# Kernel optimization log

Measured on AMD Instinct MI355X. Metric: run time of the kernel, lower is better.

## Reference

```python
import jax, jax.numpy as jnp
import numpy as np

N = 30000      # nodes
E = 1000000    # edges
G = 256        # graphs
IN = 3         # in_channels
H = 8          # heads
D = 16         # per-head dim
HID = 128      # hidden_dim = H*D
L = 3          # num_layers
KP = 17        # num_keypoints
KPE = 16       # kp_emb_dim
NEG = 0.2      # GATv2 leaky_relu negative slope
EPS = 1e-5     # BatchNorm eps


def setup_inputs() -> dict:
    key = jax.random.key(0)
    ks = jax.random.split(key, 24)
    x = jax.random.normal(ks[0], (N, IN), jnp.float32)
    edge_index = jax.random.randint(ks[1], (2, E), 0, N, jnp.int32)
    batch = jnp.sort(jax.random.randint(ks[2], (N,), 0, G, jnp.int32))
    s_in = 1.0 / np.sqrt(IN + KPE)
    s_h = 1.0 / np.sqrt(HID)
    return {
        "x": x,
        "edge_index": edge_index,
        "batch": batch,
        "kp_emb": jax.random.normal(ks[3], (KP, KPE), jnp.float32),
        "w_in": jax.random.normal(ks[4], (IN + KPE, HID), jnp.float32) * s_in,
        "b_in": jax.random.normal(ks[5], (HID,), jnp.float32) * 0.01,
        "w_l": jax.random.normal(ks[6], (L, HID, HID), jnp.float32) * s_h,
        "w_r": jax.random.normal(ks[7], (L, HID, HID), jnp.float32) * s_h,
        "att": jax.random.normal(ks[8], (L, H, D), jnp.float32) * (1.0 / np.sqrt(D)),
        "conv_bias": jax.random.normal(ks[9], (L, HID), jnp.float32) * 0.01,
        "bn_gamma": jnp.ones((L, HID), jnp.float32) + 0.1 * jax.random.normal(ks[10], (L, HID), jnp.float32),
        "bn_beta": 0.1 * jax.random.normal(ks[11], (L, HID), jnp.float32),
        "bn_mean": 0.1 * jax.random.normal(ks[12], (L, HID), jnp.float32),
        "bn_var": 0.5 + jax.random.uniform(ks[13], (L, HID), jnp.float32),
        "w1": jax.random.normal(ks[14], (HID, 2 * HID), jnp.float32) * s_h,
        "b1": jnp.zeros((2 * HID,), jnp.float32),
        "w2": jax.random.normal(ks[15], (2 * HID, HID), jnp.float32) * (1.0 / np.sqrt(2 * HID)),
        "b2": jnp.zeros((HID,), jnp.float32),
        "w3": jax.random.normal(ks[16], (HID, 2), jnp.float32) * s_h,
        "b3": jnp.zeros((2,), jnp.float32),
    }


def reference(x, edge_index, batch, kp_emb, w_in, b_in, w_l, w_r, att, conv_bias,
              bn_gamma, bn_beta, bn_mean, bn_var, w1, b1, w2, b2, w3, b3):
    n = x.shape[0]
    # keypoint id embedding concat + input projection
    kp_ids = jnp.arange(n) % KP
    h = jnp.concatenate([x, kp_emb[kp_ids]], axis=-1) @ w_in + b_in  # [N, HID]
    # GATv2Conv adds self loops by default
    loops = jnp.arange(n, dtype=edge_index.dtype)
    src = jnp.concatenate([edge_index[0], loops])  # message sources (j)
    dst = jnp.concatenate([edge_index[1], loops])  # message targets (i)
    for l in range(L):
        xl = (h @ w_l[l]).reshape(n, H, D)  # source transform (lin_l)
        xr = (h @ w_r[l]).reshape(n, H, D)  # target transform (lin_r)
        z = xl[src] + xr[dst]                              # [Et, H, D]
        score = jnp.einsum('ehd,hd->eh', jax.nn.leaky_relu(z, NEG), att[l])
        # segment softmax over incoming edges of each dst node
        m = jax.ops.segment_max(score, dst, num_segments=n)
        ex = jnp.exp(score - m[dst])
        denom = jax.ops.segment_sum(ex, dst, num_segments=n)
        alpha = ex / denom[dst]                            # [Et, H]
        msg = xl[src] * alpha[..., None]                   # [Et, H, D]
        out = jax.ops.segment_sum(msg, dst, num_segments=n).reshape(n, HID) + conv_bias[l]
        out = jax.nn.relu(out)
        # BatchNorm1d (eval mode: running stats)
        out = (out - bn_mean[l]) * (bn_gamma[l] / jnp.sqrt(bn_var[l] + EPS)) + bn_beta[l]
        h = h + out  # residual (dropout = identity in eval)
    # global mean pool per graph
    sums = jax.ops.segment_sum(h, batch, num_segments=G)
    cnt = jax.ops.segment_sum(jnp.ones((n, 1), h.dtype), batch, num_segments=G)
    g = sums / jnp.maximum(cnt, 1.0)
    # classifier MLP
    g = jax.nn.elu(g @ w1 + b1)
    g = jax.nn.elu(g @ w2 + b2)
    return g @ w3 + b3  # [G, 2]
```

## Files before the change

### kernel.cpp

```cpp
#include <hip/hip_runtime.h>
#include <hip/hip_bf16.h>

#define N_NODES 30000
#define N_EDGES 1000000
#define N_GRAPHS 256
#define HEADS 8
#define DHEAD 16
#define HIDDEN 128
#define LAYERS 3
#define KPN 17
#define KPE 16
#define NEG_SLOPE 0.2f
#define BN_EPS 1e-5f
#define ET (N_EDGES + N_NODES)
#define NBIN 235
#define BINW 128
#define BINCAP 6144
#define CHUNK 4096
#define NB_EDGE 245
#define NB_WCONV 384
#define SRC_HALF 15000

typedef __attribute__((ext_vector_type(8))) short bf16x8;
typedef __attribute__((ext_vector_type(4))) float f32x4;

__device__ __forceinline__ unsigned bf16_rne(float f) {
    unsigned u = __float_as_uint(f);
    return (u + 0x7fffu + ((u >> 16) & 1u)) >> 16;
}

__global__ __launch_bounds__(256) void k_bin(const int* __restrict__ ei,
                                             int* __restrict__ bcnt,
                                             unsigned* __restrict__ bdata,
                                             const int* __restrict__ batch,
                                             int* __restrict__ gptr,
                                             int* __restrict__ ptr,
                                             const float* __restrict__ w_l,
                                             const float* __restrict__ w_r,
                                             unsigned short* __restrict__ wT) {
    int bid = blockIdx.x;
    if (bid < NB_EDGE) {
        __shared__ int lcnt[NBIN];
        __shared__ int lbase[NBIN];
        int base = bid * CHUNK;
        int n = N_EDGES - base; if (n > CHUNK) n = CHUNK;
        for (int i = threadIdx.x; i < NBIN; i += 256) lcnt[i] = 0;
        __syncthreads();
        for (int t = threadIdx.x; t < n; t += 256) {
            int d = ei[N_EDGES + base + t];
            atomicAdd(&lcnt[d >> 7], 1);
        }
        __syncthreads();
        for (int i = threadIdx.x; i < NBIN; i += 256) {
            int c = lcnt[i];
            lbase[i] = c ? atomicAdd(&bcnt[i], c) : 0;
            lcnt[i] = 0;
        }
        __syncthreads();
        for (int t = threadIdx.x; t < n; t += 256) {
            int s = ei[base + t];
            int d = ei[N_EDGES + base + t];
            int b = d >> 7;
            int pos = lbase[b] + atomicAdd(&lcnt[b], 1);
            bdata[(size_t)b * BINCAP + pos] = (unsigned)s | ((unsigned)(d & 127) << 15);
        }
    } else if (bid == NB_EDGE) {
        for (int g = threadIdx.x; g <= N_GRAPHS; g += 256) {
            if (g == N_GRAPHS) { gptr[g] = N_NODES; }
            else {
                int lo = 0, hi = N_NODES;
                while (lo < hi) {
                    int mid = (lo + hi) >> 1;
                    if (batch[mid] < g) lo = mid + 1; else hi = mid;
                }
                gptr[g] = lo;
            }
        }
        if (threadIdx.x == 0) ptr[N_NODES] = ET;
    } else {
        int idx = (bid - NB_EDGE - 1) * 256 + threadIdx.x;
        if (idx < LAYERS * 256 * 128) {
            int l = idx / (256 * 128);
            int rem = idx - l * 256 * 128;
            int c = rem >> 7;
            int k = rem & 127;
            float v = (c < 128) ? w_l[(size_t)l * 16384 + k * 128 + c]
                                : w_r[(size_t)l * 16384 + k * 128 + (c - 128)];
            wT[idx] = (unsigned short)bf16_rne(v);
        }
    }
}

__global__ __launch_bounds__(256) void k_place2(const int* __restrict__ bcnt,
                                                const unsigned* __restrict__ bdata,
                                                int* __restrict__ ptr,
                                                unsigned short* __restrict__ csr_src) {
    __shared__ int vsc[256];
    __shared__ int histL[BINW], histH[BINW];
    __shared__ int lowS[BINW], highS[BINW];
    __shared__ int lofsL[BINW], lofsH[BINW];
    __shared__ int bbase_sh;
    int b = blockIdx.x, tid = threadIdx.x;

    int c = 0;
    if (tid < NBIN) {
        int nodes = N_NODES - tid * BINW; if (nodes > BINW) nodes = BINW;
        c = bcnt[tid] + nodes;
    }
    vsc[tid] = c;
    __syncthreads();
    for (int off = 1; off < 256; off <<= 1) {
        int x = (tid >= off) ? vsc[tid - off] : 0;
        __syncthreads();
        vsc[tid] += x;
        __syncthreads();
    }
    if (tid == 0) bbase_sh = (b == 0) ? 0 : vsc[b - 1];

    int nNodes = N_NODES - b * BINW; if (nNodes > BINW) nNodes = BINW;
    int n = bcnt[b];
    if (tid < BINW) {
        int node = b * BINW + tid;
        int valid = tid < nNodes;
        histL[tid] = (valid && node < SRC_HALF) ? 1 : 0;
        histH[tid] = (valid && node >= SRC_HALF) ? 1 : 0;
    }
    __syncthreads();
    for (int t = tid; t < n; t += 256) {
        unsigned e = bdata[(size_t)b * BINCAP + t];
        int dl = (e >> 15) & 127;
        if ((e & 0x7fffu) < SRC_HALF) atomicAdd(&histL[dl], 1);
        else                          atomicAdd(&histH[dl], 1);
    }
    __syncthreads();
    if (tid < BINW) vsc[tid] = histL[tid] + histH[tid];
    __syncthreads();
    for (int off = 1; off < BINW; off <<= 1) {
        int x = (tid >= off && tid < BINW) ? vsc[tid - off] : 0;
        __syncthreads();
        if (tid < BINW) vsc[tid] += x;
        __syncthreads();
    }
    if (tid < BINW) {
        int tot = histL[tid] + histH[tid];
        int ns = bbase_sh + vsc[tid] - tot;
        lowS[tid] = ns;
        highS[tid] = ns + histL[tid];
        int node = b * BINW + tid;
        int isLow = node < SRC_HALF;
        if (tid < nNodes) {
            ptr[node] = ns;
            if (isLow) csr_src[ns] = (unsigned short)node;
            else       csr_src[ns + histL[tid]] = (unsigned short)node;
        }
        lofsL[tid] = (tid < nNodes && isLow) ? 1 : 0;
        lofsH[tid] = (tid < nNodes && !isLow) ? 1 : 0;
    }
    __syncthreads();
    for (int t = tid; t < n; t += 256) {
        unsigned e = bdata[(size_t)b * BINCAP + t];
        int dl = (e >> 15) & 127;
        int s = e & 0x7fffu;
        int pos = (s < SRC_HALF) ? (lowS[dl] + atomicAdd(&lofsL[dl], 1))
                                 : (highS[dl] + atomicAdd(&lofsH[dl], 1));
        csr_src[pos] = (unsigned short)s;
    }
}

template<bool FUSED>
__global__ __launch_bounds__(256) void k_gemmT(const float* __restrict__ x,
                                               const float* __restrict__ kp_emb,
                                               const float* __restrict__ w_in,
                                               const float* __restrict__ b_in,
                                               float* __restrict__ h,
                                               const unsigned short* __restrict__ hb,
                                               const unsigned short* __restrict__ wT,
                                               unsigned short* __restrict__ xlb,
                                               unsigned short* __restrict__ xrb) {
    __shared__ unsigned short hsA[32][136];
    __shared__ unsigned short st[32][264];
    int tid = threadIdx.x;
    int wave = tid >> 6, lane = tid & 63;
    int brow = blockIdx.x * 32;
    int lr = lane & 15, lk = lane >> 4;

    if (FUSED) {
        int r = tid >> 3, c16 = (tid & 7) * 16;
        int gr = brow + r;
        int gc = gr < N_NODES ? gr : 0;
        float xv0 = x[gc * 3], xv1 = x[gc * 3 + 1], xv2 = x[gc * 3 + 2];
        const float* kp = kp_emb + (gc % KPN) * KPE;
        float res[16];
#pragma unroll
        for (int q = 0; q < 16; ++q) {
            int c = c16 + q;
            float acc = b_in[c] + xv0 * w_in[c] + xv1 * w_in[128 + c] + xv2 * w_in[256 + c];
#pragma unroll
            for (int kk = 0; kk < KPE; ++kk) acc += kp[kk] * w_in[(3 + kk) * 128 + c];
            res[q] = acc;
        }
        if (gr < N_NODES) {
#pragma unroll
            for (int q = 0; q < 16; q += 4)
                *(float4*)(h + (size_t)gr * 128 + c16 + q) =
                    make_float4(res[q], res[q + 1], res[q + 2], res[q + 3]);
        }
#pragma unroll
        for (int q = 0; q < 16; ++q) hsA[r][c16 + q] = (unsigned short)bf16_rne(res[q]);
        __syncthreads();
    }

    int ar0c = brow + lr;      if (ar0c >= N_NODES) ar0c = N_NODES - 1;
    int ar1c = brow + 16 + lr; if (ar1c >= N_NODES) ar1c = N_NODES - 1;
    int c0 = wave * 64 + lr;
    const unsigned short* wb = wT + (size_t)c0 * 128 + lk * 8;

    f32x4 acc[2][4];
#pragma unroll
    for (int m = 0; m < 2; ++m)
#pragma unroll
        for (int n = 0; n < 4; ++n) acc[m][n] = (f32x4){0.f, 0.f, 0.f, 0.f};

#pragma unroll
    for (int ks = 0; ks < 4; ++ks) {
        bf16x8 a0, a1;
        if (FUSED) {
            a0 = *(const bf16x8*)&hsA[lr][lk * 8 + ks * 32];
            a1 = *(const bf16x8*)&hsA[16 + lr][lk * 8 + ks * 32];
        } else {
            a0 = *(const bf16x8*)(hb + (size_t)ar0c * 128 + lk * 8 + ks * 32);
            a1 = *(const bf16x8*)(hb + (size_t)ar1c * 128 + lk * 8 + ks * 32);
        }
#pragma unroll
        for (int nt = 0; nt < 4; ++nt) {
            bf16x8 b = *(const bf16x8*)(wb + nt * 16 * 128 + ks * 32);
            acc[0][nt] = __builtin_amdgcn_mfma_f32_16x16x32_bf16(a0, b, acc[0][nt], 0, 0, 0);
            acc[1][nt] = __builtin_amdgcn_mfma_f32_16x16x32_bf16(a1, b, acc[1][nt], 0, 0, 0);
        }
    }

    int r0 = lk * 4;
#pragma unroll
    for (int mt = 0; mt < 2; ++mt)
#pragma unroll
        for (int nt = 0; nt < 4; ++nt)
#pragma unroll
            for (int j = 0; j < 4; ++j)
                st[r0 + mt * 16 + j][c0 + nt * 16] = (unsigned short)bf16_rne(acc[mt][nt][j]);
    __syncthreads();

    int rr = tid >> 3, seg = tid & 7;
    int grow = brow + rr;
    if (grow < N_NODES) {
        uint4 v0 = *(uint4*)&st[rr][seg * 32];
        uint4 v1 = *(uint4*)&st[rr][seg * 32 + 8];
        uint4 v2 = *(uint4*)&st[rr][seg * 32 + 16];
        uint4 v3 = *(uint4*)&st[rr][seg * 32 + 24];
        unsigned short* dst = (seg < 4) ? (xlb + (size_t)grow * 128 + seg * 32)
                                        : (xrb + (size_t)grow * 128 + (seg - 4) * 32);
        *(uint4*)(dst)      = v0;
        *(uint4*)(dst + 8)  = v1;
        *(uint4*)(dst + 16) = v2;
        *(uint4*)(dst + 24) = v3;
    }
}

__global__ __launch_bounds__(256) void k_gat(const unsigned* __restrict__ xlb,
                                             const unsigned* __restrict__ xrb,
                                             const int* __restrict__ ptr,
                                             const unsigned short* __restrict__ csr_src,
                                             const float* __restrict__ att_l,
                                             const float* __restrict__ bias_l,
                                             const float* __restrict__ gamma_l,
                                             const float* __restrict__ beta_l,
                                             const float* __restrict__ mean_l,
                                             const float* __restrict__ var_l,
                                             float* __restrict__ h,
                                             unsigned short* __restrict__ hb) {
    int wid = (blockIdx.x * 256 + threadIdx.x) >> 6;
    int lane = threadIdx.x & 63;
    if (wid >= N_NODES) return;
    int i = wid;
    int grp = lane >> 5;
    int l32 = lane & 31;
    int d0 = 4 * l32;

    uint2 xw = *(const uint2*)(xrb + ((size_t)i << 6) + (l32 << 1));
    float xr0 = __uint_as_float(xw.x << 16);
    float xr1 = __uint_as_float(xw.x & 0xffff0000u);
    float xr2 = __uint_as_float(xw.y << 16);
    float xr3 = __uint_as_float(xw.y & 0xffff0000u);
    const float L2E = 1.44269504089f;
    float4 av = *(const float4*)(att_l + d0);
    av.x *= L2E; av.y *= L2E; av.z *= L2E; av.w *= L2E;
    int e0 = ptr[i], e1 = ptr[i + 1];

    float denom = 0.f, acc0 = 0.f, acc1 = 0.f, acc2 = 0.f, acc3 = 0.f;

#define LDP(KP, WREG, VREG) { \
    int eo = 2 * (KP) + grp; \
    int sr = __shfl(sv, eo); \
    VREG = eo < cnt; \
    int rw = VREG ? sr : 0; \
    WREG = *(const uint2*)(xlb + ((size_t)rw << 6) + (l32 << 1)); \
}
#define PROCP(WREG, VREG) { \
    float v0 = __uint_as_float(WREG.x << 16); \
    float v1 = __uint_as_float(WREG.x & 0xffff0000u); \
    float v2 = __uint_as_float(WREG.y << 16); \
    float v3 = __uint_as_float(WREG.y & 0xffff0000u); \
    float z0 = v0 + xr0, z1 = v1 + xr1, z2 = v2 + xr2, z3 = v3 + xr3; \
    z0 = fmaxf(z0, NEG_SLOPE * z0); \
    z1 = fmaxf(z1, NEG_SLOPE * z1); \
    z2 = fmaxf(z2, NEG_SLOPE * z2); \
    z3 = fmaxf(z3, NEG_SLOPE * z3); \
    float p = z0 * av.x + z1 * av.y + z2 * av.z + z3 * av.w; \
    p += __shfl_xor(p, 1); \
    p += __shfl_xor(p, 2); \
    float ex = VREG ? exp2f(p) : 0.f; \
    denom += ex; \
    acc0 += ex * v0; acc1 += ex * v1; acc2 += ex * v2; acc3 += ex * v3; \
}

    for (int base = e0; base < e1; base += 64) {
        int idx = base + lane;
        int sv = (idx < e1) ? (int)csr_src[idx] : 0;
        int cnt = e1 - base; if (cnt > 64) cnt = 64;
        int np = (cnt + 1) >> 1;

        uint2 w0, w1; bool b0 = false, b1 = false;
        LDP(0, w0, b0);
        if (1 < np) LDP(1, w1, b1);
        int k = 0;
        for (; k + 2 < np; k += 2) {
            uint2 n0, n1; bool c0v, c1v;
            LDP(k + 2, n0, c0v);
            LDP(k + 3, n1, c1v);
            PROCP(w0, b0); PROCP(w1, b1);
            w0 = n0; b0 = c0v; w1 = n1; b1 = c1v;
        }
        PROCP(w0, b0);
        if (k + 1 < np) PROCP(w1, b1);
    }
#undef LDP
#undef PROCP

    denom += __shfl_xor(denom, 32);
    acc0 += __shfl_xor(acc0, 32);
    acc1 += __shfl_xor(acc1, 32);
    acc2 += __shfl_xor(acc2, 32);
    acc3 += __shfl_xor(acc3, 32);

    if (grp == 0) {
        float inv = 1.f / denom;
        float4 bia = *(const float4*)(bias_l + d0);
        float4 gam = *(const float4*)(gamma_l + d0);
        float4 bet = *(const float4*)(beta_l + d0);
        float4 mea = *(const float4*)(mean_l + d0);
        float4 var = *(const float4*)(var_l + d0);
        float o0 = fmaxf(acc0 * inv + bia.x, 0.f);
        float o1 = fmaxf(acc1 * inv + bia.y, 0.f);
        float o2 = fmaxf(acc2 * inv + bia.z, 0.f);
        float o3 = fmaxf(acc3 * inv + bia.w, 0.f);
        o0 = (o0 - mea.x) * (gam.x * rsqrtf(var.x + BN_EPS)) + bet.x;
        o1 = (o1 - mea.y) * (gam.y * rsqrtf(var.y + BN_EPS)) + bet.y;
        o2 = (o2 - mea.z) * (gam.z * rsqrtf(var.z + BN_EPS)) + bet.z;
        o3 = (o3 - mea.w) * (gam.w * rsqrtf(var.w + BN_EPS)) + bet.w;
        float4 hv = *(const float4*)(h + (size_t)i * 128 + d0);
        hv.x += o0; hv.y += o1; hv.z += o2; hv.w += o3;
        *(float4*)(h + (size_t)i * 128 + d0) = hv;
        unsigned pk0 = bf16_rne(hv.x) | (bf16_rne(hv.y) << 16);
        unsigned pk1 = bf16_rne(hv.z) | (bf16_rne(hv.w) << 16);
        uint2 pk; pk.x = pk0; pk.y = pk1;
        *(uint2*)(hb + (size_t)i * 128 + d0) = pk;
    }
}

__global__ __launch_bounds__(256) void k_poolmlp(const float* __restrict__ h,
                                                 const int* __restrict__ gptr,
                                                 const float* __restrict__ w1, const float* __restrict__ b1,
                                                 const float* __restrict__ w2, const float* __restrict__ b2,
                                                 const float* __restrict__ w3, const float* __restrict__ b3,
                                                 float* __restrict__ out) {
    __shared__ float red[256];
    __shared__ float g[128], t1[256], t2[128];
    int b = blockIdx.x, t = threadIdx.x;
    int c = t & 127, half = t >> 7;
    int lo = gptr[b], hi = gptr[b + 1];
    float s = 0.f;
    for (int i = lo + half; i < hi; i += 2) s += h[(size_t)i * 128 + c];
    red[t] = s;
    __syncthreads();
    if (half == 0) {
        float cntf = fmaxf((float)(hi - lo), 1.0f);
        g[c] = (red[c] + red[c + 128]) / cntf;
    }
    __syncthreads();
    {
        float acc = b1[t];
        for (int k = 0; k < 128; ++k) acc += g[k] * w1[k * 256 + t];
        t1[t] = acc > 0.f ? acc : expm1f(acc);
    }
    __syncthreads();
    if (t < 128) {
        float acc = b2[t];
        for (int k = 0; k < 256; ++k) acc += t1[k] * w2[k * 128 + t];
        t2[t] = acc > 0.f ? acc : expm1f(acc);
    }
    __syncthreads();
    if (t < 2) {
        float acc = b3[t];
        for (int k = 0; k < 128; ++k) acc += t2[k] * w3[k * 2 + t];
        out[b * 2 + t] = acc;
    }
}

extern "C" void kernel_launch(void* const* d_in, const int* in_sizes, int n_in,
                              void* d_out, int out_size, void* d_ws, size_t ws_size,
                              hipStream_t stream) {
    const float* x        = (const float*)d_in[0];
    const int*   ei       = (const int*)d_in[1];
    const int*   batch    = (const int*)d_in[2];
    const float* kp_emb   = (const float*)d_in[3];
    const float* w_in     = (const float*)d_in[4];
    const float* b_in     = (const float*)d_in[5];
    const float* w_l      = (const float*)d_in[6];
    const float* w_r      = (const float*)d_in[7];
    const float* att      = (const float*)d_in[8];
    const float* conv_b   = (const float*)d_in[9];
    const float* bn_gamma = (const float*)d_in[10];
    const float* bn_beta  = (const float*)d_in[11];
    const float* bn_mean  = (const float*)d_in[12];
    const float* bn_var   = (const float*)d_in[13];
    const float* w1 = (const float*)d_in[14];
    const float* b1 = (const float*)d_in[15];
    const float* w2 = (const float*)d_in[16];
    const float* b2 = (const float*)d_in[17];
    const float* w3 = (const float*)d_in[18];
    const float* b3 = (const float*)d_in[19];
    float* out = (float*)d_out;

    char* ws = (char*)d_ws;
    const size_t OFF_H    = 0;
    const size_t OFF_HB   = OFF_H    + 15360000;
    const size_t OFF_XL   = OFF_HB   + 7680000;
    const size_t OFF_XR   = OFF_XL   + 7680000;
    const size_t OFF_WT   = OFF_XR   + 7680000;
    const size_t OFF_PTR  = OFF_WT   + 196608;
    const size_t OFF_BCNT = OFF_PTR  + 120320;
    const size_t OFF_SRC  = OFF_BCNT + 1024;
    const size_t OFF_GPTR = OFF_SRC  + 2060032;

    float*          h      = (float*)(ws + OFF_H);
    unsigned short* hb     = (unsigned short*)(ws + OFF_HB);
    unsigned short* xlb    = (unsigned short*)(ws + OFF_XL);
    unsigned short* xrb    = (unsigned short*)(ws + OFF_XR);
    unsigned*       bdata  = (unsigned*)(ws + OFF_XR);
    unsigned short* wT     = (unsigned short*)(ws + OFF_WT);
    int*            ptr    = (int*)(ws + OFF_PTR);
    int*            bcnt   = (int*)(ws + OFF_BCNT);
    unsigned short* csrsrc = (unsigned short*)(ws + OFF_SRC);
    int*            gptr   = (int*)(ws + OFF_GPTR);

    hipMemsetAsync(bcnt, 0, NBIN * 4, stream);
    k_bin<<<NB_EDGE + 1 + NB_WCONV, 256, 0, stream>>>(ei, bcnt, bdata, batch, gptr, ptr,
                                                      w_l, w_r, wT);
    k_place2<<<NBIN, 256, 0, stream>>>(bcnt, bdata, ptr, csrsrc);

    for (int l = 0; l < LAYERS; ++l) {
        const unsigned short* wTl = wT + (size_t)l * 256 * 128;
        if (l == 0)
            k_gemmT<true><<<(N_NODES + 31) / 32, 256, 0, stream>>>(
                x, kp_emb, w_in, b_in, h, hb, wTl, xlb, xrb);
        else
            k_gemmT<false><<<(N_NODES + 31) / 32, 256, 0, stream>>>(
                x, kp_emb, w_in, b_in, h, hb, wTl, xlb, xrb);
        k_gat<<<(N_NODES + 3) / 4, 256, 0, stream>>>(
            (const unsigned*)xlb, (const unsigned*)xrb, ptr, csrsrc,
            att + (size_t)l * 128, conv_b + (size_t)l * 128,
            bn_gamma + (size_t)l * 128, bn_beta + (size_t)l * 128,
            bn_mean + (size_t)l * 128, bn_var + (size_t)l * 128, h, hb);
    }

    k_poolmlp<<<N_GRAPHS, 256, 0, stream>>>(h, gptr, w1, b1, w2, b2, w3, b3, out);
}
```

Baseline: 272.1 us.

## Overlap edge binning with layer-0 GEMM and stage CSR placement in LDS

Edge binning moves out of the preprocessing kernel into extra blocks of the layer-0 fused GEMM launch, so binning runs concurrently with the first projection. bdata gets its own workspace region because it no longer aliases xrb. bcnt is zeroed in the new k_pre kernel, which replaces the memset. k_place2 now loads each bin into shared memory, drops the low/high source-half split, builds the CSR segment locally, and writes it out contiguously. The intent is to cut launches and serial preprocessing and to turn scattered global writes into coalesced ones. The cost is heavier LDS use per block (about 38 KB) and more LDS in the GEMM kernel, which may lower occupancy. Dropping the source-half ordering may also change gather locality in k_gat.

```diff
diff --git a/kernel.cpp b/kernel.cpp
--- a/kernel.cpp
+++ b/kernel.cpp
@@ -18,8 +18,7 @@
 #define BINCAP 6144
 #define CHUNK 4096
 #define NB_EDGE 245
-#define NB_WCONV 384
-#define SRC_HALF 15000
+#define NBGEMM 938
 
 typedef __attribute__((ext_vector_type(8))) short bf16x8;
 typedef __attribute__((ext_vector_type(4))) float f32x4;
@@ -29,43 +28,17 @@
     return (u + 0x7fffu + ((u >> 16) & 1u)) >> 16;
 }
 
-__global__ __launch_bounds__(256) void k_bin(const int* __restrict__ ei,
+__global__ __launch_bounds__(256) void k_pre(const int* __restrict__ batch,
                                              int* __restrict__ bcnt,
-                                             unsigned* __restrict__ bdata,
-                                             const int* __restrict__ batch,
                                              int* __restrict__ gptr,
                                              int* __restrict__ ptr,
                                              const float* __restrict__ w_l,
                                              const float* __restrict__ w_r,
                                              unsigned short* __restrict__ wT) {
-    int bid = blockIdx.x;
-    if (bid < NB_EDGE) {
-        __shared__ int lcnt[NBIN];
-        __shared__ int lbase[NBIN];
-        int base = bid * CHUNK;
-        int n = N_EDGES - base; if (n > CHUNK) n = CHUNK;
-        for (int i = threadIdx.x; i < NBIN; i += 256) lcnt[i] = 0;
-        __syncthreads();
-        for (int t = threadIdx.x; t < n; t += 256) {
-            int d = ei[N_EDGES + base + t];
-            atomicAdd(&lcnt[d >> 7], 1);
-        }
-        __syncthreads();
-        for (int i = threadIdx.x; i < NBIN; i += 256) {
-            int c = lcnt[i];
-            lbase[i] = c ? atomicAdd(&bcnt[i], c) : 0;
-            lcnt[i] = 0;
-        }
-        __syncthreads();
-        for (int t = threadIdx.x; t < n; t += 256) {
-            int s = ei[base + t];
-            int d = ei[N_EDGES + base + t];
-            int b = d >> 7;
-            int pos = lbase[b] + atomicAdd(&lcnt[b], 1);
-            bdata[(size_t)b * BINCAP + pos] = (unsigned)s | ((unsigned)(d & 127) << 15);
-        }
-    } else if (bid == NB_EDGE) {
-        for (int g = threadIdx.x; g <= N_GRAPHS; g += 256) {
+    int bid = blockIdx.x, t = threadIdx.x;
+    if (bid == 0) {
+        if (t < NBIN) bcnt[t] = 0;
+        for (int g = t; g <= N_GRAPHS; g += 256) {
             if (g == N_GRAPHS) { gptr[g] = N_NODES; }
             else {
                 int lo = 0, hi = N_NODES;
@@ -76,9 +49,9 @@
                 gptr[g] = lo;
             }
         }
-        if (threadIdx.x == 0) ptr[N_NODES] = ET;
+        if (t == 0) ptr[N_NODES] = ET;
     } else {
-        int idx = (bid - NB_EDGE - 1) * 256 + threadIdx.x;
+        int idx = (bid - 1) * 256 + t;
         if (idx < LAYERS * 256 * 128) {
             int l = idx / (256 * 128);
             int rem = idx - l * 256 * 128;
@@ -88,82 +61,6 @@
                                 : w_r[(size_t)l * 16384 + k * 128 + (c - 128)];
             wT[idx] = (unsigned short)bf16_rne(v);
         }
-    }
-}
-
-__global__ __launch_bounds__(256) void k_place2(const int* __restrict__ bcnt,
-                                                const unsigned* __restrict__ bdata,
-                                                int* __restrict__ ptr,
-                                                unsigned short* __restrict__ csr_src) {
-    __shared__ int vsc[256];
-    __shared__ int histL[BINW], histH[BINW];
-    __shared__ int lowS[BINW], highS[BINW];
-    __shared__ int lofsL[BINW], lofsH[BINW];
-    __shared__ int bbase_sh;
-    int b = blockIdx.x, tid = threadIdx.x;
-
-    int c = 0;
-    if (tid < NBIN) {
-        int nodes = N_NODES - tid * BINW; if (nodes > BINW) nodes = BINW;
-        c = bcnt[tid] + nodes;
-    }
-    vsc[tid] = c;
-    __syncthreads();
-    for (int off = 1; off < 256; off <<= 1) {
-        int x = (tid >= off) ? vsc[tid - off] : 0;
-        __syncthreads();
-        vsc[tid] += x;
-        __syncthreads();
-    }
-    if (tid == 0) bbase_sh = (b == 0) ? 0 : vsc[b - 1];
-
-    int nNodes = N_NODES - b * BINW; if (nNodes > BINW) nNodes = BINW;
-    int n = bcnt[b];
-    if (tid < BINW) {
-        int node = b * BINW + tid;
-        int valid = tid < nNodes;
-        histL[tid] = (valid && node < SRC_HALF) ? 1 : 0;
-        histH[tid] = (valid && node >= SRC_HALF) ? 1 : 0;
-    }
-    __syncthreads();
-    for (int t = tid; t < n; t += 256) {
-        unsigned e = bdata[(size_t)b * BINCAP + t];
-        int dl = (e >> 15) & 127;
-        if ((e & 0x7fffu) < SRC_HALF) atomicAdd(&histL[dl], 1);
-        else                          atomicAdd(&histH[dl], 1);
-    }
-    __syncthreads();
-    if (tid < BINW) vsc[tid] = histL[tid] + histH[tid];
-    __syncthreads();
-    for (int off = 1; off < BINW; off <<= 1) {
-        int x = (tid >= off && tid < BINW) ? vsc[tid - off] : 0;
-        __syncthreads();
-        if (tid < BINW) vsc[tid] += x;
-        __syncthreads();
-    }
-    if (tid < BINW) {
-        int tot = histL[tid] + histH[tid];
-        int ns = bbase_sh + vsc[tid] - tot;
-        lowS[tid] = ns;
-        highS[tid] = ns + histL[tid];
-        int node = b * BINW + tid;
-        int isLow = node < SRC_HALF;
-        if (tid < nNodes) {
-            ptr[node] = ns;
-            if (isLow) csr_src[ns] = (unsigned short)node;
-            else       csr_src[ns + histL[tid]] = (unsigned short)node;
-        }
-        lofsL[tid] = (tid < nNodes && isLow) ? 1 : 0;
-        lofsH[tid] = (tid < nNodes && !isLow) ? 1 : 0;
-    }
-    __syncthreads();
-    for (int t = tid; t < n; t += 256) {
-        unsigned e = bdata[(size_t)b * BINCAP + t];
-        int dl = (e >> 15) & 127;
-        int s = e & 0x7fffu;
-        int pos = (s < SRC_HALF) ? (lowS[dl] + atomicAdd(&lofsL[dl], 1))
-                                 : (highS[dl] + atomicAdd(&lofsH[dl], 1));
-        csr_src[pos] = (unsigned short)s;
     }
 }
 
@@ -176,10 +73,42 @@
                                                const unsigned short* __restrict__ hb,
                                                const unsigned short* __restrict__ wT,
                                                unsigned short* __restrict__ xlb,
-                                               unsigned short* __restrict__ xrb) {
+                                               unsigned short* __restrict__ xrb,
+                                               const int* __restrict__ ei,
+                                               int* __restrict__ bcnt,
+                                               unsigned* __restrict__ bdata) {
     __shared__ unsigned short hsA[32][136];
     __shared__ unsigned short st[32][264];
+    __shared__ int lcnt[NBIN];
+    __shared__ int lbase[NBIN];
     int tid = threadIdx.x;
+
+    if (FUSED && blockIdx.x >= NBGEMM) {
+        int base = (blockIdx.x - NBGEMM) * CHUNK;
+        int n = N_EDGES - base; if (n > CHUNK) n = CHUNK;
+        for (int i = tid; i < NBIN; i += 256) lcnt[i] = 0;
+        __syncthreads();
+        for (int t = tid; t < n; t += 256) {
+            int d = ei[N_EDGES + base + t];
+            atomicAdd(&lcnt[d >> 7], 1);
+        }
+        __syncthreads();
+        for (int i = tid; i < NBIN; i += 256) {
+            int c = lcnt[i];
+            lbase[i] = c ? atomicAdd(&bcnt[i], c) : 0;
+            lcnt[i] = 0;
+        }
+        __syncthreads();
+        for (int t = tid; t < n; t += 256) {
+            int s = ei[base + t];
+            int d = ei[N_EDGES + base + t];
+            int b = d >> 7;
+            int pos = lbase[b] + atomicAdd(&lcnt[b], 1);
+            bdata[(size_t)b * BINCAP + pos] = (unsigned)s | ((unsigned)(d & 127) << 15);
+        }
+        return;
+    }
+
     int wave = tid >> 6, lane = tid & 63;
     int brow = blockIdx.x * 32;
     int lr = lane & 15, lk = lane >> 4;
@@ -263,6 +192,70 @@
         *(uint4*)(dst + 16) = v2;
         *(uint4*)(dst + 24) = v3;
     }
+}
+
+__global__ __launch_bounds__(256) void k_place2(const int* __restrict__ bcnt,
+                                                const unsigned* __restrict__ bdata,
+                                                int* __restrict__ ptr,
+                                                unsigned short* __restrict__ csr_src) {
+    __shared__ int vsc[256];
+    __shared__ unsigned ldata[BINCAP];
+    __shared__ unsigned short lcsr[BINCAP + BINW];
+    __shared__ int hist[BINW], pre[BINW], nodestart[BINW], lofs[BINW];
+    __shared__ int bbase_sh;
+    int b = blockIdx.x, tid = threadIdx.x;
+    int n = bcnt[b];
+    int nNodes = N_NODES - b * BINW; if (nNodes > BINW) nNodes = BINW;
+
+    for (int t = tid; t < n; t += 256) ldata[t] = bdata[(size_t)b * BINCAP + t];
+
+    int c = 0;
+    if (tid < NBIN) {
+        int nodes = N_NODES - tid * BINW; if (nodes > BINW) nodes = BINW;
+        c = bcnt[tid] + nodes;
+    }
+    vsc[tid] = c;
+    if (tid < BINW) hist[tid] = (tid < nNodes) ? 1 : 0;
+    __syncthreads();
+    for (int off = 1; off < 256; off <<= 1) {
+        int x = (tid >= off) ? vsc[tid - off] : 0;
+        __syncthreads();
+        vsc[tid] += x;
+        __syncthreads();
+    }
+    if (tid == 0) bbase_sh = (b == 0) ? 0 : vsc[b - 1];
+
+    for (int t = tid; t < n; t += 256)
+        atomicAdd(&hist[(ldata[t] >> 15) & 127], 1);
+    __syncthreads();
+    if (tid < BINW) pre[tid] = hist[tid];
+    __syncthreads();
+    for (int off = 1; off < BINW; off <<= 1) {
+        int x = (tid >= off && tid < BINW) ? pre[tid - off] : 0;
+        __syncthreads();
+        if (tid < BINW) pre[tid] += x;
+        __syncthreads();
+    }
+    if (tid < BINW) {
+        int ns = pre[tid] - hist[tid];
+        nodestart[tid] = ns;
+        if (tid < nNodes) {
+            int node = b * BINW + tid;
+            ptr[node] = bbase_sh + ns;
+            lcsr[ns] = (unsigned short)node;
+        }
+        lofs[tid] = 1;
+    }
+    __syncthreads();
+    for (int t = tid; t < n; t += 256) {
+        unsigned e = ldata[t];
+        int dl = (e >> 15) & 127;
+        int pos = nodestart[dl] + atomicAdd(&lofs[dl], 1);
+        lcsr[pos] = (unsigned short)(e & 0x7fffu);
+    }
+    __syncthreads();
+    int tot = n + nNodes;
+    for (int t = tid; t < tot; t += 256) csr_src[bbase_sh + t] = lcsr[t];
 }
 
 __global__ __launch_bounds__(256) void k_gat(const unsigned* __restrict__ xlb,
@@ -450,31 +443,33 @@
     const size_t OFF_BCNT = OFF_PTR  + 120320;
     const size_t OFF_SRC  = OFF_BCNT + 1024;
     const size_t OFF_GPTR = OFF_SRC  + 2060032;
+    const size_t OFF_BD   = OFF_GPTR + 1088;
 
     float*          h      = (float*)(ws + OFF_H);
     unsigned short* hb     = (unsigned short*)(ws + OFF_HB);
     unsigned short* xlb    = (unsigned short*)(ws + OFF_XL);
     unsigned short* xrb    = (unsigned short*)(ws + OFF_XR);
-    unsigned*       bdata  = (unsigned*)(ws + OFF_XR);
     unsigned short* wT     = (unsigned short*)(ws + OFF_WT);
     int*            ptr    = (int*)(ws + OFF_PTR);
     int*            bcnt   = (int*)(ws + OFF_BCNT);
     unsigned short* csrsrc = (unsigned short*)(ws + OFF_SRC);
     int*            gptr   = (int*)(ws + OFF_GPTR);
-
-    hipMemsetAsync(bcnt, 0, NBIN * 4, stream);
-    k_bin<<<NB_EDGE + 1 + NB_WCONV, 256, 0, stream>>>(ei, bcnt, bdata, batch, gptr, ptr,
-                                                      w_l, w_r, wT);
+    unsigned*       bdata  = (unsigned*)(ws + OFF_BD);
+
+    k_pre<<<1 + (LAYERS * 256 * 128 + 255) / 256, 256, 0, stream>>>(
+        batch, bcnt, gptr, ptr, w_l, w_r, wT);
+
+    k_gemmT<true><<<NBGEMM + NB_EDGE, 256, 0, stream>>>(
+        x, kp_emb, w_in, b_in, h, hb, wT, xlb, xrb, ei, bcnt, bdata);
+
     k_place2<<<NBIN, 256, 0, stream>>>(bcnt, bdata, ptr, csrsrc);
 
     for (int l = 0; l < LAYERS; ++l) {
-        const unsigned short* wTl = wT + (size_t)l * 256 * 128;
-        if (l == 0)
-            k_gemmT<true><<<(N_NODES + 31) / 32, 256, 0, stream>>>(
-                x, kp_emb, w_in, b_in, h, hb, wTl, xlb, xrb);
-        else
-            k_gemmT<false><<<(N_NODES + 31) / 32, 256, 0, stream>>>(
-                x, kp_emb, w_in, b_in, h, hb, wTl, xlb, xrb);
+        if (l > 0) {
+            k_gemmT<false><<<NBGEMM, 256, 0, stream>>>(
+                x, kp_emb, w_in, b_in, h, hb, wT + (size_t)l * 256 * 128, xlb, xrb,
+                ei, bcnt, bdata);
+        }
         k_gat<<<(N_NODES + 3) / 4, 256, 0, stream>>>(
             (const unsigned*)xlb, (const unsigned*)xrb, ptr, csrsrc,
             att + (size_t)l * 128, conv_b + (size_t)l * 128,
```

Result: faster. 255.7 us (-6.0%).
